# Optimization experiments

Hardware: AMD Instinct MI355X
Metric: run time of the kernel (lower is better)

The kernel has to match this reference:

```python
import jax, jax.numpy as jnp
import numpy as np

B, T, N, D = 8, 512, 64, 128
PRED, HEADS, HID = 96, 8, 256
KERNELS = (17, 49)
NUM_LAYERS = 1
NUM_BLOCKS = 1
IDX_T = np.arange(64)   # lowest 64 of T//2=256 rfft modes (mode_select='low')
IDX_C = np.arange(32)   # min(modes, (N+1)//2)=32 lowest channel-frequency modes


def _mov_avg(x, k):
    # x: [B, T, N]; replicate-pad (k-1)//2 on both ends, then box filter (AvgPool1d stride 1)
    pad = (k - 1) // 2
    xp = jnp.concatenate([jnp.repeat(x[:, :1], pad, axis=1), x, jnp.repeat(x[:, -1:], pad, axis=1)], axis=1)
    c = jnp.cumsum(xp, axis=1)
    c = jnp.concatenate([jnp.zeros_like(c[:, :1]), c], axis=1)
    return (c[:, k:] - c[:, :-k]) / k


def _decomp_multi(x, dec_w, dec_b):
    # series_decomp_multi: softmax-weighted mixture of moving averages
    mm = jnp.stack([_mov_avg(x, k) for k in KERNELS], axis=-1)        # [B,T,N,K]
    w = jax.nn.softmax(x[..., None] * dec_w + dec_b, axis=-1)         # Linear(1,K) on x, softmax over K
    trend = jnp.sum(mm * w, axis=-1)
    return x - trend, trend


def _complex_attn(x, Wq, Wk, Wv, Wo):
    # x: complex64 [B, L, M, D]; multi-head attention over the M selected frequency modes.
    # Real projection weights applied to complex activations; attention weights are
    # softmax over |q k^H| / sqrt(dh); values stay complex.
    Bq, L, M, Dm = x.shape
    dh = Dm // HEADS
    q = jnp.einsum('blmd,de->blme', x, Wq).reshape(Bq, L, M, HEADS, dh)
    k = jnp.einsum('blmd,de->blme', x, Wk).reshape(Bq, L, M, HEADS, dh)
    v = jnp.einsum('blmd,de->blme', x, Wv).reshape(Bq, L, M, HEADS, dh)
    s = jnp.einsum('blmhd,blnhd->blhmn', q, jnp.conj(k))              # complex scores
    w = jax.nn.softmax(jnp.abs(s) / np.sqrt(dh), axis=-1)             # real attn weights
    o = jnp.einsum('blhmn,blnhd->blmhd', w.astype(x.dtype), v).reshape(Bq, L, M, Dm)
    return jnp.einsum('blmd,de->blme', o, Wo)


def _cem(x, Wq, Wk, Wv, Wo):
    # channel-frequency attention; x: [B, N, T, D]
    xp = jnp.transpose(x, (0, 2, 1, 3))                               # [B,T,N,D]
    xf = jnp.fft.rfft(xp, axis=2)                                     # [B,T,N//2+1,D]
    xs = xf[:, :, IDX_C, :]                                           # gather selected modes
    for _ in range(NUM_LAYERS):
        xs = _complex_attn(xs, Wq, Wk, Wv, Wo)
    yf = jnp.zeros((x.shape[0], T, N // 2 + 1, D), dtype=xf.dtype).at[:, :, IDX_C, :].set(xs)
    y = jnp.fft.irfft(yf, n=N, axis=2)
    return jnp.transpose(y, (0, 2, 1, 3))


def _tem(x, Wq, Wk, Wv, Wo):
    # temporal-frequency attention; x: [B, N, T, D]
    xf = jnp.fft.rfft(x, axis=2)                                      # [B,N,T//2+1,D]
    xs = xf[:, :, IDX_T, :]
    for _ in range(NUM_LAYERS):
        xs = _complex_attn(xs, Wq, Wk, Wv, Wo)
    yf = jnp.zeros((x.shape[0], N, T // 2 + 1, D), dtype=xf.dtype).at[:, :, IDX_T, :].set(xs)
    return jnp.fft.irfft(yf, n=T, axis=2)


def setup_inputs() -> dict:
    key = jax.random.key(0)
    ks = jax.random.split(key, 24)
    r = lambda i, shape, s: jax.random.normal(ks[i], shape, jnp.float32) * s
    K = len(KERNELS)
    return {
        'x': jax.random.normal(ks[0], (B, T, N), jnp.float32),
        'embeddings': jax.random.normal(ks[1], (1, D), jnp.float32),
        'dec_w': r(2, (K,), 1.0),
        'dec_b': jnp.zeros((K,), jnp.float32),
        'mlp_w1': r(3, (T, HID), 1.0 / np.sqrt(T)),
        'mlp_b1': jnp.zeros((HID,), jnp.float32),
        'mlp_w2': r(4, (HID, HID), 1.0 / np.sqrt(HID)),
        'mlp_b2': jnp.zeros((HID,), jnp.float32),
        'mlp_w3': r(5, (HID, PRED), 1.0 / np.sqrt(HID)),
        'mlp_b3': jnp.zeros((PRED,), jnp.float32),
        'cem_Wq': r(6, (D, D), 0.02), 'cem_Wk': r(7, (D, D), 0.02),
        'cem_Wv': r(8, (D, D), 0.02), 'cem_Wo': r(9, (D, D), 0.02),
        'tem_Wq': r(10, (D, D), 0.02), 'tem_Wk': r(11, (D, D), 0.02),
        'tem_Wv': r(12, (D, D), 0.02), 'tem_Wo': r(13, (D, D), 0.02),
        'dr_w': r(14, (D, 1), 1.0 / np.sqrt(D)),
        'dr_b': jnp.zeros((1,), jnp.float32),
        'out_w': r(15, (T, PRED), 1.0 / np.sqrt(T)),
        'out_b': jnp.zeros((PRED,), jnp.float32),
        'W_fuse': jnp.ones((2,), jnp.float32),
    }


def reference(x, embeddings, dec_w, dec_b, mlp_w1, mlp_b1, mlp_w2, mlp_b2, mlp_w3, mlp_b3,
              cem_Wq, cem_Wk, cem_Wv, cem_Wo, tem_Wq, tem_Wk, tem_Wv, tem_Wo,
              dr_w, dr_b, out_w, out_b, W_fuse):
    res, trend = _decomp_multi(x, dec_w, dec_b)
    t = jnp.transpose(trend, (0, 2, 1))                               # [B,N,T]
    h = jax.nn.relu(t @ mlp_w1 + mlp_b1)
    h = jax.nn.relu(h @ mlp_w2 + mlp_b2)
    trend_out = jnp.transpose(h @ mlp_w3 + mlp_b3, (0, 2, 1))         # [B,PRED,N]
    # tokenEmb: [B,T,N] -> [B,N,T,1] * [1,D]
    xe = jnp.transpose(res, (0, 2, 1))[..., None] * embeddings[0]      # [B,N,T,D]
    for _ in range(NUM_BLOCKS):
        xe = _cem(xe, cem_Wq, cem_Wk, cem_Wv, cem_Wo)
    for _ in range(NUM_BLOCKS):
        xe = _tem(xe, tem_Wq, tem_Wk, tem_Wv, tem_Wo)
    xr = jnp.einsum('bntd,do->bnto', xe, dr_w)[..., 0] + dr_b[0]      # dim_reduction -> [B,N,T]
    xo = jnp.transpose(jnp.einsum('bnt,tp->bnp', xr, out_w) + out_b, (0, 2, 1))  # [B,PRED,N]
    return W_fuse[0] * xo + W_fuse[1] * trend_out
```

## Files before the change

kernel.cpp:

```cpp
#include <hip/hip_runtime.h>
#include <hip/hip_bf16.h>

typedef __hip_bfloat16 bf16;

constexpr int CB = 8;
constexpr int CT = 512;
constexpr int CN = 64;
constexpr int CD = 128;
constexpr int CP = 96;
constexpr int CH = 8;
constexpr int CDH = 16;
constexpr int CHID = 256;
constexpr int CM = 32;
constexpr int CG = 64;
constexpr float TWO_PI = 6.28318530717958647692f;

__device__ __forceinline__ float LD(const void* p, size_t i, bool f) {
  return f ? ((const float*)p)[i] : __bfloat162float(((const bf16*)p)[i]);
}
template <bool F32>
__device__ __forceinline__ float LDT(const void* p, size_t i) {
  return F32 ? ((const float*)p)[i] : __bfloat162float(((const bf16*)p)[i]);
}

__device__ __forceinline__ bool detect_f32(const void* x) {
  const unsigned int* xw = (const unsigned int*)x;
  unsigned int w = xw[threadIdx.x & 63];
  unsigned int e = (w >> 7) & 0xFF;
  unsigned long long m = __ballot(e >= 0x90 || e <= 0x60);
  return __popcll(m) > 3;
}

__device__ __forceinline__ float2 pkfma(float2 a, float2 b, float2 c) {
  return make_float2(fmaf(a.x, b.x, c.x), fmaf(a.y, b.y, c.y));
}

__global__ __launch_bounds__(256) void kL1(const void* x, const void* dec_w, const void* dec_b,
                                           const void* out_w, const void* emb, const void* cWq,
                                           const void* cWk, const void* cWv, const void* cWo,
                                           const void* tWo, const void* drw,
                                           float* res, float* trend, float* owr, float* owi,
                                           float* g_ch, float* g_ewo, float* g_wod) {
  __shared__ float sm[CT * 17];
  bool f32 = detect_f32(x);
  int blk = blockIdx.x, tid = threadIdx.x;
  if (blk < 32) {
    float (*xl)[17] = (float (*)[17])sm;
    int b = blk >> 2, n0 = (blk & 3) * 16;
    size_t base = (size_t)b * CT * CN + n0;
    for (int i = tid; i < CT * 16; i += 256) {
      int t = i >> 4, j = i & 15;
      xl[t][j] = LD(x, base + (size_t)t * CN + j, f32);
    }
    __syncthreads();
    float w0 = LD(dec_w, 0, f32), w1 = LD(dec_w, 1, f32);
    float c0 = LD(dec_b, 0, f32), c1 = LD(dec_b, 1, f32);
    int j = tid & 15, tl = tid >> 4;
    for (int k = 0; k < CT / 16; ++k) {
      int t = k * 16 + tl;
      float s17 = 0;
      #pragma unroll
      for (int o = -8; o <= 8; ++o) {
        int u = t + o; u = u < 0 ? 0 : (u > CT - 1 ? CT - 1 : u);
        s17 += xl[u][j];
      }
      float s49 = 0;
      #pragma unroll
      for (int o = -24; o <= 24; ++o) {
        int u = t + o; u = u < 0 ? 0 : (u > CT - 1 ? CT - 1 : u);
        s49 += xl[u][j];
      }
      float m0 = s17 * (1.f / 17.f), m1 = s49 * (1.f / 49.f);
      float xv = xl[t][j];
      float l0 = xv * w0 + c0, l1 = xv * w1 + c1;
      float mx = fmaxf(l0, l1);
      float e0 = __expf(l0 - mx), e1 = __expf(l1 - mx);
      float tr = (e0 * m0 + e1 * m1) / (e0 + e1);
      size_t o = ((size_t)(b * CT + t)) * CN + n0 + j;
      trend[o] = tr;
      res[o] = xv - tr;
    }
  } else if (blk < 96) {
    float* twc = sm; float* tws = sm + CT;
    int g = blk - 32;
    for (int t = tid; t < CT; t += 256) {
      int k = (g * t) & (CT - 1);
      float s, c;
      sincosf((float)k * (TWO_PI / CT), &s, &c);
      twc[t] = c; tws[t] = s;
    }
    __syncthreads();
    if (tid < CP) {
      float sr = 0, si = 0;
      #pragma unroll 8
      for (int t = 0; t < CT; ++t) {
        float w = LD(out_w, t * CP + tid, f32);
        sr += w * twc[t]; si += w * tws[t];
      }
      owr[g * CP + tid] = sr; owi[g * CP + tid] = si;
    }
  } else {
    float* eml = sm; float* drl = sm + 128; float* eql = sm + 256;
    float* ekl = sm + 384; float* evl = sm + 512;
    if (tid < 128) eml[tid] = LD(emb, tid, f32);
    else drl[tid - 128] = LD(drw, tid - 128, f32);
    __syncthreads();
    int e = tid & 127;
    for (int pass = 0; pass < 2; ++pass) {
      int grp = pass * 2 + (tid >> 7);
      if (grp < 3) {
        const void* W = grp == 0 ? cWq : (grp == 1 ? cWk : cWv);
        float a = 0;
        #pragma unroll 8
        for (int d = 0; d < CD; ++d) a += eml[d] * LD(W, d * CD + e, f32);
        (grp == 0 ? eql : (grp == 1 ? ekl : evl))[e] = a;
      } else {
        float a = 0;
        #pragma unroll 8
        for (int d = 0; d < CD; ++d) a += LD(tWo, e * CD + d, f32) * drl[d];
        g_wod[e] = a;
      }
    }
    __syncthreads();
    if (tid < CH) {
      float c = 0;
      for (int j = 0; j < CDH; ++j) c += eql[tid * CDH + j] * ekl[tid * CDH + j];
      g_ch[tid] = fabsf(c);
    }
    int half = tid >> 7;
    for (int hh = 0; hh < 4; ++hh) {
      int h = half * 4 + hh;
      float a = 0;
      #pragma unroll
      for (int j = 0; j < CDH; ++j) a += evl[h * CDH + j] * LD(cWo, (h * CDH + j) * CD + e, f32);
      g_ewo[h * CD + e] = a;
    }
  }
}

template <bool F32>
__device__ __forceinline__ void k2_body(float* sm, const float* __restrict__ trend, const void* w1,
                                        const void* bb1, const void* w2, const void* bb2,
                                        const void* w3, const void* bb3,
                                        float* __restrict__ trendo) {
  float* rows = sm;
  float* h1 = sm + 2048;
  float* h2 = sm + 3072;
  int r0 = blockIdx.x * 4;
  int b = r0 >> 6, n0 = r0 & 63;
  int tid = threadIdx.x;
  const float* tb = trend + (size_t)b * CT * CN + n0;
  for (int i = tid; i < 4 * CT; i += 256) {
    int q = i & 3, t = i >> 2;
    rows[q * CT + t] = tb[(size_t)t * CN + q];
  }
  __syncthreads();
  int c = tid;
  float a0, a1, a2, a3;
  {
    float bias = LDT<F32>(bb1, c);
    a0 = a1 = a2 = a3 = 0.f;
    #pragma unroll 16
    for (int t = 0; t < CT; ++t) {
      float w = LDT<F32>(w1, t * CHID + c);
      a0 += rows[0 * CT + t] * w; a1 += rows[1 * CT + t] * w;
      a2 += rows[2 * CT + t] * w; a3 += rows[3 * CT + t] * w;
    }
    h1[0 * CHID + c] = fmaxf(a0 + bias, 0.f); h1[1 * CHID + c] = fmaxf(a1 + bias, 0.f);
    h1[2 * CHID + c] = fmaxf(a2 + bias, 0.f); h1[3 * CHID + c] = fmaxf(a3 + bias, 0.f);
  }
  __syncthreads();
  {
    float bias = LDT<F32>(bb2, c);
    a0 = a1 = a2 = a3 = 0.f;
    #pragma unroll 16
    for (int i = 0; i < CHID; ++i) {
      float w = LDT<F32>(w2, i * CHID + c);
      a0 += h1[0 * CHID + i] * w; a1 += h1[1 * CHID + i] * w;
      a2 += h1[2 * CHID + i] * w; a3 += h1[3 * CHID + i] * w;
    }
    h2[0 * CHID + c] = fmaxf(a0 + bias, 0.f); h2[1 * CHID + c] = fmaxf(a1 + bias, 0.f);
    h2[2 * CHID + c] = fmaxf(a2 + bias, 0.f); h2[3 * CHID + c] = fmaxf(a3 + bias, 0.f);
  }
  __syncthreads();
  if (tid < 2 * CP) {
    int p = tid < CP ? tid : tid - CP;
    int qh = tid < CP ? 0 : 2;
    float bias = LDT<F32>(bb3, p);
    a0 = a1 = 0.f;
    #pragma unroll 16
    for (int i = 0; i < CHID; ++i) {
      float w = LDT<F32>(w3, i * CP + p);
      a0 += h2[qh * CHID + i] * w; a1 += h2[(qh + 1) * CHID + i] * w;
    }
    trendo[((size_t)(b * CN + n0 + qh)) * CP + p] = a0 + bias;
    trendo[((size_t)(b * CN + n0 + qh + 1)) * CP + p] = a1 + bias;
  }
}

__global__ __launch_bounds__(256) void kL2(const void* x, const float* trend, const void* w1,
                                           const void* bb1, const void* w2, const void* bb2,
                                           const void* w3, const void* bb3, float* trendo,
                                           const float* res, const float* g_ch, float* P,
                                           const void* tWq, const void* tWk, const void* tWv,
                                           const float* g_ewo, float* g_ewq, float* g_ewk,
                                           float* g_ewv) {
  __shared__ float sm[4096];
  bool f32 = detect_f32(x);
  int blk = blockIdx.x, tid = threadIdx.x;
  if (blk < 128) {
    if (f32) k2_body<true>(sm, trend, w1, bb1, w2, bb2, w3, bb3, trendo);
    else     k2_body<false>(sm, trend, w1, bb1, w2, bb2, w3, bb3, trendo);
  } else if (blk < 1152) {
    float* rowl = sm;
    float* twc = sm + 256;
    float* tws = sm + 320;
    float* chl = sm + 384;
    float* Rr = sm + 392;
    float* Ri = sm + 520;
    float* aR = sm + 648;
    float* Sr = sm + 776;
    float* Si = sm + 1800;
    int tblk = blk - 128;
    int b = tblk >> 7;
    int w = tid >> 6, lane = tid & 63;
    int t = ((tblk & 127) << 2) + w;
    rowl[w * 64 + lane] = res[((size_t)(b * CT + t)) * CN + lane];
    if (w == 0) {
      float s, c;
      sincosf((float)lane * (TWO_PI / CN), &s, &c);
      twc[lane] = c; tws[lane] = s;
    }
    if (tid < CH) chl[tid] = g_ch[tid];
    __syncthreads();
    if (lane < CM) {
      float rr = 0, ri = 0;
      int idx = 0;
      for (int n2 = 0; n2 < CN; ++n2) {
        rr += rowl[w * 64 + n2] * twc[idx];
        ri -= rowl[w * 64 + n2] * tws[idx];
        idx = (idx + lane) & (CN - 1);
      }
      Rr[w * 32 + lane] = rr; Ri[w * 32 + lane] = ri;
      aR[w * 32 + lane] = sqrtf(rr * rr + ri * ri);
    }
    __syncthreads();
    float amax = 0;
    for (int m = 0; m < CM; ++m) amax = fmaxf(amax, aR[w * 32 + m]);
    for (int i = 0; i < 4; ++i) {
      int pair = lane + 64 * i;
      int h = pair >> 5, m = pair & 31;
      float alpha = 0.25f * chl[h] * aR[w * 32 + m];
      float den = 0, sr = 0, si = 0;
      for (int n2 = 0; n2 < CM; ++n2) {
        float e = __expf(alpha * (aR[w * 32 + n2] - amax));
        den += e; sr += e * Rr[w * 32 + n2]; si += e * Ri[w * 32 + n2];
      }
      Sr[w * 256 + pair] = sr / den; Si[w * 256 + pair] = si / den;
    }
    __syncthreads();
    int n2 = lane;
    float av[8];
    for (int h = 0; h < CH; ++h) {
      float a = Sr[w * 256 + h * CM];
      int idx = n2 & (CN - 1);
      #pragma unroll
      for (int f = 1; f < CM; ++f) {
        a += 2.f * (Sr[w * 256 + h * CM + f] * twc[idx] - Si[w * 256 + h * CM + f] * tws[idx]);
        idx = (idx + n2) & (CN - 1);
      }
      av[h] = a * (1.f / CN);
    }
    float* Pb = P + (((size_t)(b * CN + n2)) * CT + t) * CH;
    ((float4*)Pb)[0] = make_float4(av[0], av[1], av[2], av[3]);
    ((float4*)Pb)[1] = make_float4(av[4], av[5], av[6], av[7]);
  } else {
    float* ew = sm;
    int pairIdx = (blk - 1152) * 2 + (tid >> 7);
    int which = pairIdx >> 3, h = pairIdx & 7, e = tid & 127;
    ew[(tid >> 7) * 128 + e] = g_ewo[h * CD + e];
    __syncthreads();
    const void* W = which == 0 ? tWq : (which == 1 ? tWk : tWv);
    float a = 0;
    #pragma unroll 8
    for (int d = 0; d < CD; ++d) a += ew[(tid >> 7) * 128 + d] * LD(W, d * CD + e, f32);
    (which == 0 ? g_ewq : (which == 1 ? g_ewk : g_ewv))[h * CD + e] = a;
  }
}

__global__ __launch_bounds__(256) void kL3(const float* P, float* Q, const float* g_ewq,
                                           const float* g_ewk, const float* g_ewv,
                                           const float* g_wod, float* g_C, float* g_u) {
  __shared__ float sm[4096];
  int blk = blockIdx.x, tid = threadIdx.x;
  if (blk < 512) {
    float* Pl = sm;
    int b = blk >> 6, n = blk & 63;
    const float4* Pp4 = (const float4*)(P + ((size_t)(b * CN + n)) * CT * CH);
    float4* Pl4 = (float4*)Pl;
    for (int i = tid; i < CT * CH / 4; i += 256) Pl4[i] = Pp4[i];
    __syncthreads();
    int g1 = tid >> 3, h = tid & 7, g2 = g1 + 32;
    float s1, c1, s2, c2;
    sincosf((float)g1 * (TWO_PI / CT), &s1, &c1);
    sincosf((float)g2 * (TWO_PI / CT), &s2, &c2);
    float wr1 = 1.f, wi1 = 0.f, wr2 = 1.f, wi2 = 0.f;
    float r1 = 0, i1 = 0, r2 = 0, i2 = 0;
    #pragma unroll 8
    for (int t = 0; t < CT; ++t) {
      float p = Pl[t * CH + h];
      r1 += p * wr1; i1 += p * wi1;
      r2 += p * wr2; i2 += p * wi2;
      float nr1 = wr1 * c1 + wi1 * s1; wi1 = wi1 * c1 - wr1 * s1; wr1 = nr1;
      float nr2 = wr2 * c2 + wi2 * s2; wi2 = wi2 * c2 - wr2 * s2; wr2 = nr2;
    }
    float* Qb = Q + ((size_t)(b * CN + n)) * CG * CH * 2;
    Qb[(g1 * CH + h) * 2] = r1; Qb[(g1 * CH + h) * 2 + 1] = i1;
    Qb[(g2 * CH + h) * 2] = r2; Qb[(g2 * CH + h) * 2 + 1] = i2;
  } else {
    for (int id = tid; id < 512 + 64; id += 256) {
      if (id < 512) {
        int h = id >> 6, a = (id >> 3) & 7, b2 = id & 7;
        float c = 0;
        #pragma unroll
        for (int j = 0; j < CDH; ++j)
          c += g_ewq[a * CD + h * CDH + j] * g_ewk[b2 * CD + h * CDH + j];
        g_C[id] = c;
      } else {
        int r = id - 512;
        int h = r >> 3, a = r & 7;
        float c = 0;
        #pragma unroll
        for (int j = 0; j < CDH; ++j) c += g_ewv[a * CD + h * CDH + j] * g_wod[h * CDH + j];
        g_u[r] = c;
      }
    }
  }
}

__global__ __launch_bounds__(512) void k5_tem(const void* x, const float* Q, const float* g_C,
                                              const float* g_u, const float* owr,
                                              const float* owi, const float* trendo,
                                              const void* dr_b, const void* out_b,
                                              const void* wfuse, void* out) {
  __shared__ float QL[CG][16];
  __shared__ float Cl[512];
  __shared__ float Ul[CH][8];
  __shared__ float2 vdL[CH][CG];
  __shared__ float2 zL[CH][CG];
  __shared__ float zrow[CG][2];
  bool f32 = detect_f32(x);
  int blk = blockIdx.x;
  int b = blk >> 6, n = blk & 63;
  int tid = threadIdx.x;
  const float* Qb = Q + ((size_t)(b * CN + n)) * CG * CH * 2;
  ((float2*)&QL[0][0])[tid] = ((const float2*)Qb)[tid];
  Cl[tid] = g_C[tid];
  if (tid < 64) ((float*)Ul)[tid] = g_u[tid];
  __syncthreads();
  int h = tid >> 6, m = tid & 63;
  float2 qp[8];
  {
    const float4* q4 = (const float4*)QL[m];
    #pragma unroll
    for (int j = 0; j < 4; ++j) {
      float4 y = q4[j];
      qp[2 * j] = make_float2(y.x, y.y);
      qp[2 * j + 1] = make_float2(y.z, y.w);
    }
  }
  {
    float vr = 0, vi = 0;
    #pragma unroll
    for (int a = 0; a < 8; ++a) { float u = Ul[h][a]; vr += qp[a].x * u; vi += qp[a].y * u; }
    vdL[h][m] = make_float2(vr, vi);
  }
  float2 uu[8], vv[8];
  #pragma unroll
  for (int bb = 0; bb < 8; ++bb) {
    float sr = 0, si = 0;
    #pragma unroll
    for (int a = 0; a < 8; ++a) {
      float c = Cl[(h * 8 + a) * 8 + bb];
      sr += qp[a].x * c; si += qp[a].y * c;
    }
    uu[bb] = make_float2(sr, si);
    vv[bb] = make_float2(si, -sr);
  }
  __syncthreads();
  float mx = -1e30f, den = 0.f, zr = 0.f, zi = 0.f;
  #pragma unroll 4
  for (int g = 0; g < CG; ++g) {
    const float4* k4p = (const float4*)QL[g];
    float2 sr2 = make_float2(0.f, 0.f), si2 = make_float2(0.f, 0.f);
    #pragma unroll
    for (int j = 0; j < 4; ++j) {
      float4 y = k4p[j];
      float2 y0 = make_float2(y.x, y.y), y1 = make_float2(y.z, y.w);
      sr2 = pkfma(uu[2 * j], y0, sr2); si2 = pkfma(vv[2 * j], y0, si2);
      sr2 = pkfma(uu[2 * j + 1], y1, sr2); si2 = pkfma(vv[2 * j + 1], y1, si2);
    }
    float sr = sr2.x + sr2.y;
    float si = si2.x + si2.y;
    float s = 0.25f * sqrtf(sr * sr + si * si);
    if (s > mx) {
      float f = __expf(mx - s);
      den *= f; zr *= f; zi *= f; mx = s;
    }
    float e = __expf(s - mx);
    float2 vd = vdL[h][g];
    den += e; zr += e * vd.x; zi += e * vd.y;
  }
  float rv = 1.f / den;
  zL[h][m] = make_float2(zr * rv, zi * rv);
  __syncthreads();
  if (tid < 128) {
    int g = tid >> 1, c = tid & 1;
    float a = 0;
    #pragma unroll
    for (int hh = 0; hh < CH; ++hh) a += c ? zL[hh][g].y : zL[hh][g].x;
    zrow[g][c] = a;
  }
  __syncthreads();
  if (tid < CP) {
    int p = tid;
    float acc = zrow[0][0] * owr[p] - zrow[0][1] * owi[p];
    #pragma unroll 8
    for (int g = 1; g < CG; ++g)
      acc += 2.f * (zrow[g][0] * owr[g * CP + p] - zrow[g][1] * owi[g * CP + p]);
    float xo = acc * (1.f / CT) + LD(dr_b, 0, f32) * owr[p] + LD(out_b, p, f32);
    float val = LD(wfuse, 0, f32) * xo + LD(wfuse, 1, f32) * trendo[((size_t)(b * CN + n)) * CP + p];
    size_t oidx = ((size_t)(b * CP + p)) * CN + n;
    if (f32) ((float*)out)[oidx] = val;
    else ((bf16*)out)[oidx] = __float2bfloat16(val);
  }
}

extern "C" void kernel_launch(void* const* d_in, const int* in_sizes, int n_in,
                              void* d_out, int out_size, void* d_ws, size_t ws_size,
                              hipStream_t stream) {
  const void* x = d_in[0];
  const void* emb = d_in[1];
  const void* dec_w = d_in[2];
  const void* dec_b = d_in[3];
  const void* mlp_w1 = d_in[4];
  const void* mlp_b1 = d_in[5];
  const void* mlp_w2 = d_in[6];
  const void* mlp_b2 = d_in[7];
  const void* mlp_w3 = d_in[8];
  const void* mlp_b3 = d_in[9];
  const void* cWq = d_in[10];
  const void* cWk = d_in[11];
  const void* cWv = d_in[12];
  const void* cWo = d_in[13];
  const void* tWq = d_in[14];
  const void* tWk = d_in[15];
  const void* tWv = d_in[16];
  const void* tWo = d_in[17];
  const void* drw = d_in[18];
  const void* drb = d_in[19];
  const void* out_w = d_in[20];
  const void* out_b = d_in[21];
  const void* wfuse = d_in[22];

  float* W = (float*)d_ws;
  float* res = W;    W += (size_t)CB * CT * CN;
  float* trend = W;  W += (size_t)CB * CT * CN;
  float* trendo = W; W += (size_t)CB * CN * CP;
  float* Pbuf = W;   W += (size_t)CB * CT * CH * CN;
  float* Qbuf = W;   W += (size_t)CB * CN * CG * CH * 2;
  float* ch = W;     W += 8;
  float* ewo = W;    W += CH * CD;
  float* ewq = W;    W += CH * CD;
  float* ewk = W;    W += CH * CD;
  float* ewv = W;    W += CH * CD;
  float* wod = W;    W += CD;
  float* owr = W;    W += CG * CP;
  float* owi = W;    W += CG * CP;
  float* gC = W;     W += 512;
  float* gU = W;     W += 64;

  kL1<<<97, 256, 0, stream>>>(x, dec_w, dec_b, out_w, emb, cWq, cWk, cWv, cWo, tWo, drw,
                              res, trend, owr, owi, ch, ewo, wod);
  kL2<<<1164, 256, 0, stream>>>(x, trend, mlp_w1, mlp_b1, mlp_w2, mlp_b2, mlp_w3, mlp_b3,
                                trendo, res, ch, Pbuf, tWq, tWk, tWv, ewo, ewq, ewk, ewv);
  kL3<<<513, 256, 0, stream>>>(Pbuf, Qbuf, ewq, ewk, ewv, wod, gC, gU);
  k5_tem<<<CB * CN, 512, 0, stream>>>(x, Qbuf, gC, gU, owr, owi, trendo, drb, out_b, wfuse,
                                      d_out);
}
```

Before: 226.3 us.

## Fuse four kernels into one cooperative persistent kernel with grid syncs

```diff
diff --git a/kernel.cpp b/kernel.cpp
--- a/kernel.cpp
+++ b/kernel.cpp
@@ -1,6 +1,8 @@
 #include <hip/hip_runtime.h>
+#include <hip/hip_cooperative_groups.h>
 #include <hip/hip_bf16.h>
 
+namespace cg = cooperative_groups;
 typedef __hip_bfloat16 bf16;
 
 constexpr int CB = 8;
@@ -35,121 +37,132 @@
   return make_float2(fmaf(a.x, b.x, c.x), fmaf(a.y, b.y, c.y));
 }
 
-__global__ __launch_bounds__(256) void kL1(const void* x, const void* dec_w, const void* dec_b,
-                                           const void* out_w, const void* emb, const void* cWq,
-                                           const void* cWk, const void* cWv, const void* cWo,
-                                           const void* tWo, const void* drw,
-                                           float* res, float* trend, float* owr, float* owi,
-                                           float* g_ch, float* g_ewo, float* g_wod) {
-  __shared__ float sm[CT * 17];
-  bool f32 = detect_f32(x);
-  int blk = blockIdx.x, tid = threadIdx.x;
+struct MArgs {
+  const void *x, *dec_w, *dec_b, *out_w, *emb, *cWq, *cWk, *cWv, *cWo;
+  const void *tWq, *tWk, *tWv, *tWo, *drw, *drb, *out_b, *wfuse;
+  const void *w1, *b1, *w2, *b2, *w3, *b3;
+  float *res, *trend, *trendo, *Pbuf, *Qbuf, *ch, *ewo, *ewq, *ewk, *ewv, *wod;
+  float *owr, *owi, *gC, *gU;
+  void* out;
+};
+
+__device__ void stage1(const MArgs& a, float* sm, bool f32, int blk, int tid) {
   if (blk < 32) {
-    float (*xl)[17] = (float (*)[17])sm;
+    float* xl = sm;
     int b = blk >> 2, n0 = (blk & 3) * 16;
     size_t base = (size_t)b * CT * CN + n0;
     for (int i = tid; i < CT * 16; i += 256) {
       int t = i >> 4, j = i & 15;
-      xl[t][j] = LD(x, base + (size_t)t * CN + j, f32);
-    }
-    __syncthreads();
-    float w0 = LD(dec_w, 0, f32), w1 = LD(dec_w, 1, f32);
-    float c0 = LD(dec_b, 0, f32), c1 = LD(dec_b, 1, f32);
+      xl[t * 16 + j] = LD(a.x, base + (size_t)t * CN + j, f32);
+    }
+    __syncthreads();
+    float w0 = LD(a.dec_w, 0, f32), w1 = LD(a.dec_w, 1, f32);
+    float c0 = LD(a.dec_b, 0, f32), c1 = LD(a.dec_b, 1, f32);
     int j = tid & 15, tl = tid >> 4;
-    for (int k = 0; k < CT / 16; ++k) {
-      int t = k * 16 + tl;
-      float s17 = 0;
-      #pragma unroll
-      for (int o = -8; o <= 8; ++o) {
-        int u = t + o; u = u < 0 ? 0 : (u > CT - 1 ? CT - 1 : u);
-        s17 += xl[u][j];
-      }
-      float s49 = 0;
-      #pragma unroll
-      for (int o = -24; o <= 24; ++o) {
-        int u = t + o; u = u < 0 ? 0 : (u > CT - 1 ? CT - 1 : u);
-        s49 += xl[u][j];
+    int t0 = tl * 32;
+    float s17 = 0.f, s49 = 0.f;
+    #pragma unroll
+    for (int o = -8; o <= 8; ++o) {
+      int u = t0 + o; u = u < 0 ? 0 : (u > CT - 1 ? CT - 1 : u);
+      s17 += xl[u * 16 + j];
+    }
+    #pragma unroll
+    for (int o = -24; o <= 24; ++o) {
+      int u = t0 + o; u = u < 0 ? 0 : (u > CT - 1 ? CT - 1 : u);
+      s49 += xl[u * 16 + j];
+    }
+    for (int k = 0; k < 32; ++k) {
+      int t = t0 + k;
+      if (k > 0) {
+        int up8 = t + 8 > CT - 1 ? CT - 1 : t + 8;
+        int dn9 = t - 9 < 0 ? 0 : t - 9;
+        int up24 = t + 24 > CT - 1 ? CT - 1 : t + 24;
+        int dn25 = t - 25 < 0 ? 0 : t - 25;
+        s17 += xl[up8 * 16 + j] - xl[dn9 * 16 + j];
+        s49 += xl[up24 * 16 + j] - xl[dn25 * 16 + j];
       }
       float m0 = s17 * (1.f / 17.f), m1 = s49 * (1.f / 49.f);
-      float xv = xl[t][j];
+      float xv = xl[t * 16 + j];
       float l0 = xv * w0 + c0, l1 = xv * w1 + c1;
       float mx = fmaxf(l0, l1);
       float e0 = __expf(l0 - mx), e1 = __expf(l1 - mx);
       float tr = (e0 * m0 + e1 * m1) / (e0 + e1);
       size_t o = ((size_t)(b * CT + t)) * CN + n0 + j;
-      trend[o] = tr;
-      res[o] = xv - tr;
+      a.trend[o] = tr;
+      a.res[o] = xv - tr;
     }
   } else if (blk < 96) {
-    float* twc = sm; float* tws = sm + CT;
+    float* ps = sm;
     int g = blk - 32;
-    for (int t = tid; t < CT; t += 256) {
-      int k = (g * t) & (CT - 1);
-      float s, c;
-      sincosf((float)k * (TWO_PI / CT), &s, &c);
-      twc[t] = c; tws[t] = s;
+    int tc = tid >> 7, idx = tid & 127;
+    if (idx < CP) {
+      int p = idx, t0 = tc * 256;
+      float s0, c0v, ss, cs;
+      sincosf((float)((g * t0) & (CT - 1)) * (TWO_PI / CT), &s0, &c0v);
+      sincosf((float)g * (TWO_PI / CT), &ss, &cs);
+      float wr = c0v, wi = s0, ar = 0.f, ai = 0.f;
+      #pragma unroll 16
+      for (int t = 0; t < 256; ++t) {
+        float w = LD(a.out_w, (size_t)(t0 + t) * CP + p, f32);
+        ar = fmaf(w, wr, ar); ai = fmaf(w, wi, ai);
+        float nr = wr * cs - wi * ss; wi = wi * cs + wr * ss; wr = nr;
+      }
+      ps[(tc * CP + p) * 2] = ar; ps[(tc * CP + p) * 2 + 1] = ai;
     }
     __syncthreads();
     if (tid < CP) {
-      float sr = 0, si = 0;
-      #pragma unroll 8
-      for (int t = 0; t < CT; ++t) {
-        float w = LD(out_w, t * CP + tid, f32);
-        sr += w * twc[t]; si += w * tws[t];
-      }
-      owr[g * CP + tid] = sr; owi[g * CP + tid] = si;
-    }
-  } else {
+      a.owr[g * CP + tid] = ps[tid * 2] + ps[(CP + tid) * 2];
+      a.owi[g * CP + tid] = ps[tid * 2 + 1] + ps[(CP + tid) * 2 + 1];
+    }
+  } else if (blk == 96) {
     float* eml = sm; float* drl = sm + 128; float* eql = sm + 256;
     float* ekl = sm + 384; float* evl = sm + 512;
-    if (tid < 128) eml[tid] = LD(emb, tid, f32);
-    else drl[tid - 128] = LD(drw, tid - 128, f32);
+    if (tid < 128) eml[tid] = LD(a.emb, tid, f32);
+    else drl[tid - 128] = LD(a.drw, tid - 128, f32);
     __syncthreads();
     int e = tid & 127;
     for (int pass = 0; pass < 2; ++pass) {
       int grp = pass * 2 + (tid >> 7);
       if (grp < 3) {
-        const void* W = grp == 0 ? cWq : (grp == 1 ? cWk : cWv);
-        float a = 0;
-        #pragma unroll 8
-        for (int d = 0; d < CD; ++d) a += eml[d] * LD(W, d * CD + e, f32);
-        (grp == 0 ? eql : (grp == 1 ? ekl : evl))[e] = a;
+        const void* W = grp == 0 ? a.cWq : (grp == 1 ? a.cWk : a.cWv);
+        float acc = 0;
+        #pragma unroll 16
+        for (int d = 0; d < CD; ++d) acc += eml[d] * LD(W, d * CD + e, f32);
+        (grp == 0 ? eql : (grp == 1 ? ekl : evl))[e] = acc;
       } else {
-        float a = 0;
-        #pragma unroll 8
-        for (int d = 0; d < CD; ++d) a += LD(tWo, e * CD + d, f32) * drl[d];
-        g_wod[e] = a;
+        float acc = 0;
+        #pragma unroll 16
+        for (int d = 0; d < CD; ++d) acc += LD(a.tWo, e * CD + d, f32) * drl[d];
+        a.wod[e] = acc;
       }
     }
     __syncthreads();
     if (tid < CH) {
       float c = 0;
       for (int j = 0; j < CDH; ++j) c += eql[tid * CDH + j] * ekl[tid * CDH + j];
-      g_ch[tid] = fabsf(c);
+      a.ch[tid] = fabsf(c);
     }
     int half = tid >> 7;
     for (int hh = 0; hh < 4; ++hh) {
       int h = half * 4 + hh;
-      float a = 0;
+      float acc = 0;
       #pragma unroll
-      for (int j = 0; j < CDH; ++j) a += evl[h * CDH + j] * LD(cWo, (h * CDH + j) * CD + e, f32);
-      g_ewo[h * CD + e] = a;
+      for (int j = 0; j < CDH; ++j)
+        acc += evl[h * CDH + j] * LD(a.cWo, (h * CDH + j) * CD + e, f32);
+      a.ewo[h * CD + e] = acc;
     }
   }
 }
 
 template <bool F32>
-__device__ __forceinline__ void k2_body(float* sm, const float* __restrict__ trend, const void* w1,
-                                        const void* bb1, const void* w2, const void* bb2,
-                                        const void* w3, const void* bb3,
-                                        float* __restrict__ trendo) {
+__device__ void k2_body(float* sm, const MArgs& a) {
   float* rows = sm;
   float* h1 = sm + 2048;
   float* h2 = sm + 3072;
   int r0 = blockIdx.x * 4;
   int b = r0 >> 6, n0 = r0 & 63;
   int tid = threadIdx.x;
-  const float* tb = trend + (size_t)b * CT * CN + n0;
+  const float* tb = a.trend + (size_t)b * CT * CN + n0;
   for (int i = tid; i < 4 * CT; i += 256) {
     int q = i & 3, t = i >> 2;
     rows[q * CT + t] = tb[(size_t)t * CN + q];
@@ -158,11 +171,11 @@
   int c = tid;
   float a0, a1, a2, a3;
   {
-    float bias = LDT<F32>(bb1, c);
+    float bias = LDT<F32>(a.b1, c);
     a0 = a1 = a2 = a3 = 0.f;
     #pragma unroll 16
     for (int t = 0; t < CT; ++t) {
-      float w = LDT<F32>(w1, t * CHID + c);
+      float w = LDT<F32>(a.w1, t * CHID + c);
       a0 += rows[0 * CT + t] * w; a1 += rows[1 * CT + t] * w;
       a2 += rows[2 * CT + t] * w; a3 += rows[3 * CT + t] * w;
     }
@@ -171,11 +184,11 @@
   }
   __syncthreads();
   {
-    float bias = LDT<F32>(bb2, c);
+    float bias = LDT<F32>(a.b2, c);
     a0 = a1 = a2 = a3 = 0.f;
     #pragma unroll 16
     for (int i = 0; i < CHID; ++i) {
-      float w = LDT<F32>(w2, i * CHID + c);
+      float w = LDT<F32>(a.w2, i * CHID + c);
       a0 += h1[0 * CHID + i] * w; a1 += h1[1 * CHID + i] * w;
       a2 += h1[2 * CHID + i] * w; a3 += h1[3 * CHID + i] * w;
     }
@@ -186,32 +199,23 @@
   if (tid < 2 * CP) {
     int p = tid < CP ? tid : tid - CP;
     int qh = tid < CP ? 0 : 2;
-    float bias = LDT<F32>(bb3, p);
+    float bias = LDT<F32>(a.b3, p);
     a0 = a1 = 0.f;
     #pragma unroll 16
     for (int i = 0; i < CHID; ++i) {
-      float w = LDT<F32>(w3, i * CP + p);
+      float w = LDT<F32>(a.w3, i * CP + p);
       a0 += h2[qh * CHID + i] * w; a1 += h2[(qh + 1) * CHID + i] * w;
     }
-    trendo[((size_t)(b * CN + n0 + qh)) * CP + p] = a0 + bias;
-    trendo[((size_t)(b * CN + n0 + qh + 1)) * CP + p] = a1 + bias;
-  }
-}
-
-__global__ __launch_bounds__(256) void kL2(const void* x, const float* trend, const void* w1,
-                                           const void* bb1, const void* w2, const void* bb2,
-                                           const void* w3, const void* bb3, float* trendo,
-                                           const float* res, const float* g_ch, float* P,
-                                           const void* tWq, const void* tWk, const void* tWv,
-                                           const float* g_ewo, float* g_ewq, float* g_ewk,
-                                           float* g_ewv) {
-  __shared__ float sm[4096];
-  bool f32 = detect_f32(x);
-  int blk = blockIdx.x, tid = threadIdx.x;
+    a.trendo[((size_t)(b * CN + n0 + qh)) * CP + p] = a0 + bias;
+    a.trendo[((size_t)(b * CN + n0 + qh + 1)) * CP + p] = a1 + bias;
+  }
+}
+
+__device__ void stage2(const MArgs& a, float* sm, bool f32, int blk, int tid) {
   if (blk < 128) {
-    if (f32) k2_body<true>(sm, trend, w1, bb1, w2, bb2, w3, bb3, trendo);
-    else     k2_body<false>(sm, trend, w1, bb1, w2, bb2, w3, bb3, trendo);
-  } else if (blk < 1152) {
+    if (f32) k2_body<true>(sm, a);
+    else     k2_body<false>(sm, a);
+  } else if (blk < 1012) {
     float* rowl = sm;
     float* twc = sm + 256;
     float* tws = sm + 320;
@@ -221,82 +225,85 @@
     float* aR = sm + 648;
     float* Sr = sm + 776;
     float* Si = sm + 1800;
-    int tblk = blk - 128;
-    int b = tblk >> 7;
+    int bk = blk - 128;
+    int iters = bk < 140 ? 2 : 1;
+    int tbase = bk < 140 ? bk * 8 : 140 * 8 + (bk - 140) * 4;
     int w = tid >> 6, lane = tid & 63;
-    int t = ((tblk & 127) << 2) + w;
-    rowl[w * 64 + lane] = res[((size_t)(b * CT + t)) * CN + lane];
     if (w == 0) {
       float s, c;
       sincosf((float)lane * (TWO_PI / CN), &s, &c);
       twc[lane] = c; tws[lane] = s;
     }
-    if (tid < CH) chl[tid] = g_ch[tid];
-    __syncthreads();
-    if (lane < CM) {
-      float rr = 0, ri = 0;
-      int idx = 0;
-      for (int n2 = 0; n2 < CN; ++n2) {
-        rr += rowl[w * 64 + n2] * twc[idx];
-        ri -= rowl[w * 64 + n2] * tws[idx];
-        idx = (idx + lane) & (CN - 1);
-      }
-      Rr[w * 32 + lane] = rr; Ri[w * 32 + lane] = ri;
-      aR[w * 32 + lane] = sqrtf(rr * rr + ri * ri);
-    }
-    __syncthreads();
-    float amax = 0;
-    for (int m = 0; m < CM; ++m) amax = fmaxf(amax, aR[w * 32 + m]);
-    for (int i = 0; i < 4; ++i) {
-      int pair = lane + 64 * i;
-      int h = pair >> 5, m = pair & 31;
-      float alpha = 0.25f * chl[h] * aR[w * 32 + m];
-      float den = 0, sr = 0, si = 0;
-      for (int n2 = 0; n2 < CM; ++n2) {
-        float e = __expf(alpha * (aR[w * 32 + n2] - amax));
-        den += e; sr += e * Rr[w * 32 + n2]; si += e * Ri[w * 32 + n2];
-      }
-      Sr[w * 256 + pair] = sr / den; Si[w * 256 + pair] = si / den;
-    }
-    __syncthreads();
-    int n2 = lane;
-    float av[8];
-    for (int h = 0; h < CH; ++h) {
-      float a = Sr[w * 256 + h * CM];
-      int idx = n2 & (CN - 1);
-      #pragma unroll
-      for (int f = 1; f < CM; ++f) {
-        a += 2.f * (Sr[w * 256 + h * CM + f] * twc[idx] - Si[w * 256 + h * CM + f] * tws[idx]);
-        idx = (idx + n2) & (CN - 1);
-      }
-      av[h] = a * (1.f / CN);
-    }
-    float* Pb = P + (((size_t)(b * CN + n2)) * CT + t) * CH;
-    ((float4*)Pb)[0] = make_float4(av[0], av[1], av[2], av[3]);
-    ((float4*)Pb)[1] = make_float4(av[4], av[5], av[6], av[7]);
+    if (tid < CH) chl[tid] = a.ch[tid];
+    __syncthreads();
+    for (int it = 0; it < iters; ++it) {
+      int task = tbase + it * 4 + w;
+      int b = task >> 9, t = task & 511;
+      rowl[w * 64 + lane] = a.res[((size_t)(b * CT + t)) * CN + lane];
+      __syncthreads();
+      if (lane < CM) {
+        float rr = 0, ri = 0;
+        int idx = 0;
+        for (int n2 = 0; n2 < CN; ++n2) {
+          rr += rowl[w * 64 + n2] * twc[idx];
+          ri -= rowl[w * 64 + n2] * tws[idx];
+          idx = (idx + lane) & (CN - 1);
+        }
+        Rr[w * 32 + lane] = rr; Ri[w * 32 + lane] = ri;
+        aR[w * 32 + lane] = sqrtf(rr * rr + ri * ri);
+      }
+      __syncthreads();
+      float amax = 0;
+      for (int m = 0; m < CM; ++m) amax = fmaxf(amax, aR[w * 32 + m]);
+      for (int i = 0; i < 4; ++i) {
+        int pair = lane + 64 * i;
+        int h = pair >> 5, m = pair & 31;
+        float alpha = 0.25f * chl[h] * aR[w * 32 + m];
+        float den = 0, sr = 0, si = 0;
+        for (int n2 = 0; n2 < CM; ++n2) {
+          float e = __expf(alpha * (aR[w * 32 + n2] - amax));
+          den += e; sr += e * Rr[w * 32 + n2]; si += e * Ri[w * 32 + n2];
+        }
+        Sr[w * 256 + pair] = sr / den; Si[w * 256 + pair] = si / den;
+      }
+      __syncthreads();
+      int n2 = lane;
+      float av[8];
+      for (int h = 0; h < CH; ++h) {
+        float acc = Sr[w * 256 + h * CM];
+        int idx = n2 & (CN - 1);
+        #pragma unroll
+        for (int f = 1; f < CM; ++f) {
+          acc += 2.f * (Sr[w * 256 + h * CM + f] * twc[idx]
+                      - Si[w * 256 + h * CM + f] * tws[idx]);
+          idx = (idx + n2) & (CN - 1);
+        }
+        av[h] = acc * (1.f / CN);
+      }
+      float* Pb = a.Pbuf + (((size_t)(b * CN + n2)) * CT + t) * CH;
+      ((float4*)Pb)[0] = make_float4(av[0], av[1], av[2], av[3]);
+      ((float4*)Pb)[1] = make_float4(av[4], av[5], av[6], av[7]);
+      __syncthreads();
+    }
   } else {
     float* ew = sm;
-    int pairIdx = (blk - 1152) * 2 + (tid >> 7);
+    int pairIdx = (blk - 1012) * 2 + (tid >> 7);
     int which = pairIdx >> 3, h = pairIdx & 7, e = tid & 127;
-    ew[(tid >> 7) * 128 + e] = g_ewo[h * CD + e];
-    __syncthreads();
-    const void* W = which == 0 ? tWq : (which == 1 ? tWk : tWv);
-    float a = 0;
-    #pragma unroll 8
-    for (int d = 0; d < CD; ++d) a += ew[(tid >> 7) * 128 + d] * LD(W, d * CD + e, f32);
-    (which == 0 ? g_ewq : (which == 1 ? g_ewk : g_ewv))[h * CD + e] = a;
-  }
-}
-
-__global__ __launch_bounds__(256) void kL3(const float* P, float* Q, const float* g_ewq,
-                                           const float* g_ewk, const float* g_ewv,
-                                           const float* g_wod, float* g_C, float* g_u) {
-  __shared__ float sm[4096];
-  int blk = blockIdx.x, tid = threadIdx.x;
+    ew[(tid >> 7) * 128 + e] = a.ewo[h * CD + e];
+    __syncthreads();
+    const void* W = which == 0 ? a.tWq : (which == 1 ? a.tWk : a.tWv);
+    float acc = 0;
+    #pragma unroll 16
+    for (int d = 0; d < CD; ++d) acc += ew[(tid >> 7) * 128 + d] * LD(W, d * CD + e, f32);
+    (which == 0 ? a.ewq : (which == 1 ? a.ewk : a.ewv))[h * CD + e] = acc;
+  }
+}
+
+__device__ void stage3(const MArgs& a, float* sm, bool f32, int blk, int tid) {
   if (blk < 512) {
     float* Pl = sm;
     int b = blk >> 6, n = blk & 63;
-    const float4* Pp4 = (const float4*)(P + ((size_t)(b * CN + n)) * CT * CH);
+    const float4* Pp4 = (const float4*)(a.Pbuf + ((size_t)(b * CN + n)) * CT * CH);
     float4* Pl4 = (float4*)Pl;
     for (int i = tid; i < CT * CH / 4; i += 256) Pl4[i] = Pp4[i];
     __syncthreads();
@@ -314,54 +321,48 @@
       float nr1 = wr1 * c1 + wi1 * s1; wi1 = wi1 * c1 - wr1 * s1; wr1 = nr1;
       float nr2 = wr2 * c2 + wi2 * s2; wi2 = wi2 * c2 - wr2 * s2; wr2 = nr2;
     }
-    float* Qb = Q + ((size_t)(b * CN + n)) * CG * CH * 2;
+    float* Qb = a.Qbuf + ((size_t)(b * CN + n)) * CG * CH * 2;
     Qb[(g1 * CH + h) * 2] = r1; Qb[(g1 * CH + h) * 2 + 1] = i1;
     Qb[(g2 * CH + h) * 2] = r2; Qb[(g2 * CH + h) * 2 + 1] = i2;
-  } else {
+  } else if (blk == 512) {
     for (int id = tid; id < 512 + 64; id += 256) {
       if (id < 512) {
-        int h = id >> 6, a = (id >> 3) & 7, b2 = id & 7;
+        int h = id >> 6, aa = (id >> 3) & 7, b2 = id & 7;
         float c = 0;
         #pragma unroll
         for (int j = 0; j < CDH; ++j)
-          c += g_ewq[a * CD + h * CDH + j] * g_ewk[b2 * CD + h * CDH + j];
-        g_C[id] = c;
+          c += a.ewq[aa * CD + h * CDH + j] * a.ewk[b2 * CD + h * CDH + j];
+        a.gC[id] = c;
       } else {
         int r = id - 512;
-        int h = r >> 3, a = r & 7;
+        int h = r >> 3, aa = r & 7;
         float c = 0;
         #pragma unroll
-        for (int j = 0; j < CDH; ++j) c += g_ewv[a * CD + h * CDH + j] * g_wod[h * CDH + j];
-        g_u[r] = c;
-      }
-    }
-  }
-}
-
-__global__ __launch_bounds__(512) void k5_tem(const void* x, const float* Q, const float* g_C,
-                                              const float* g_u, const float* owr,
-                                              const float* owi, const float* trendo,
-                                              const void* dr_b, const void* out_b,
-                                              const void* wfuse, void* out) {
-  __shared__ float QL[CG][16];
-  __shared__ float Cl[512];
-  __shared__ float Ul[CH][8];
-  __shared__ float2 vdL[CH][CG];
-  __shared__ float2 zL[CH][CG];
-  __shared__ float zrow[CG][2];
-  bool f32 = detect_f32(x);
-  int blk = blockIdx.x;
+        for (int j = 0; j < CDH; ++j) c += a.ewv[aa * CD + h * CDH + j] * a.wod[h * CDH + j];
+        a.gU[r] = c;
+      }
+    }
+  }
+}
+
+__device__ void stage4(const MArgs& a, float* sm, bool f32, int blk, int tid) {
+  if (blk >= 512) return;
+  float* QL = sm;
+  float* Cl = sm + 1024;
+  float* Ul = sm + 1536;
+  float2* vdL = (float2*)(sm + 1600);
+  float2* zL = (float2*)(sm + 2624);
+  float* zrow = sm + 3648;
   int b = blk >> 6, n = blk & 63;
-  int tid = threadIdx.x;
-  const float* Qb = Q + ((size_t)(b * CN + n)) * CG * CH * 2;
-  ((float2*)&QL[0][0])[tid] = ((const float2*)Qb)[tid];
-  Cl[tid] = g_C[tid];
-  if (tid < 64) ((float*)Ul)[tid] = g_u[tid];
-  __syncthreads();
-  int h = tid >> 6, m = tid & 63;
+  const float* Qb = a.Qbuf + ((size_t)(b * CN + n)) * CG * CH * 2;
+  for (int i = tid; i < 512; i += 256) ((float4*)QL)[i] = ((const float4*)Qb)[i];
+  for (int i = tid; i < 512; i += 256) Cl[i] = a.gC[i];
+  if (tid < 64) Ul[tid] = a.gU[tid];
+  __syncthreads();
+  int h0 = tid >> 6, m = tid & 63;
   float2 qp[8];
   {
-    const float4* q4 = (const float4*)QL[m];
+    const float4* q4 = (const float4*)(QL + m * 16);
     #pragma unroll
     for (int j = 0; j < 4; ++j) {
       float4 y = q4[j];
@@ -369,122 +370,149 @@
       qp[2 * j + 1] = make_float2(y.z, y.w);
     }
   }
-  {
+  #pragma unroll
+  for (int e2 = 0; e2 < 2; ++e2) {
+    int hh = h0 + e2 * 4;
     float vr = 0, vi = 0;
     #pragma unroll
-    for (int a = 0; a < 8; ++a) { float u = Ul[h][a]; vr += qp[a].x * u; vi += qp[a].y * u; }
-    vdL[h][m] = make_float2(vr, vi);
-  }
-  float2 uu[8], vv[8];
-  #pragma unroll
-  for (int bb = 0; bb < 8; ++bb) {
-    float sr = 0, si = 0;
+    for (int aa = 0; aa < 8; ++aa) {
+      float u = Ul[hh * 8 + aa];
+      vr += qp[aa].x * u; vi += qp[aa].y * u;
+    }
+    vdL[hh * 64 + m] = make_float2(vr, vi);
+  }
+  __syncthreads();
+  for (int e2 = 0; e2 < 2; ++e2) {
+    int hh = h0 + e2 * 4;
+    float2 uu[8], vv[8];
     #pragma unroll
-    for (int a = 0; a < 8; ++a) {
-      float c = Cl[(h * 8 + a) * 8 + bb];
-      sr += qp[a].x * c; si += qp[a].y * c;
-    }
-    uu[bb] = make_float2(sr, si);
-    vv[bb] = make_float2(si, -sr);
-  }
-  __syncthreads();
-  float mx = -1e30f, den = 0.f, zr = 0.f, zi = 0.f;
-  #pragma unroll 4
-  for (int g = 0; g < CG; ++g) {
-    const float4* k4p = (const float4*)QL[g];
-    float2 sr2 = make_float2(0.f, 0.f), si2 = make_float2(0.f, 0.f);
-    #pragma unroll
-    for (int j = 0; j < 4; ++j) {
-      float4 y = k4p[j];
-      float2 y0 = make_float2(y.x, y.y), y1 = make_float2(y.z, y.w);
-      sr2 = pkfma(uu[2 * j], y0, sr2); si2 = pkfma(vv[2 * j], y0, si2);
-      sr2 = pkfma(uu[2 * j + 1], y1, sr2); si2 = pkfma(vv[2 * j + 1], y1, si2);
-    }
-    float sr = sr2.x + sr2.y;
-    float si = si2.x + si2.y;
-    float s = 0.25f * sqrtf(sr * sr + si * si);
-    if (s > mx) {
-      float f = __expf(mx - s);
-      den *= f; zr *= f; zi *= f; mx = s;
-    }
-    float e = __expf(s - mx);
-    float2 vd = vdL[h][g];
-    den += e; zr += e * vd.x; zi += e * vd.y;
-  }
-  float rv = 1.f / den;
-  zL[h][m] = make_float2(zr * rv, zi * rv);
+    for (int bb = 0; bb < 8; ++bb) {
+      float sr = 0, si = 0;
+      #pragma unroll
+      for (int aa = 0; aa < 8; ++aa) {
+        float c = Cl[(hh * 8 + aa) * 8 + bb];
+        sr += qp[aa].x * c; si += qp[aa].y * c;
+      }
+      uu[bb] = make_float2(sr, si);
+      vv[bb] = make_float2(si, -sr);
+    }
+    float mx = -1e30f, den = 0.f, zr = 0.f, zi = 0.f;
+    #pragma unroll 4
+    for (int g = 0; g < CG; ++g) {
+      const float4* k4p = (const float4*)(QL + g * 16);
+      float2 sr2 = make_float2(0.f, 0.f), si2 = make_float2(0.f, 0.f);
+      #pragma unroll
+      for (int j = 0; j < 4; ++j) {
+        float4 y = k4p[j];
+        float2 y0 = make_float2(y.x, y.y), y1 = make_float2(y.z, y.w);
+        sr2 = pkfma(uu[2 * j], y0, sr2); si2 = pkfma(vv[2 * j], y0, si2);
+        sr2 = pkfma(uu[2 * j + 1], y1, sr2); si2 = pkfma(vv[2 * j + 1], y1, si2);
+      }
+      float sr = sr2.x + sr2.y;
+      float si = si2.x + si2.y;
+      float s = 0.25f * sqrtf(sr * sr + si * si);
+      if (s > mx) {
+        float f = __expf(mx - s);
+        den *= f; zr *= f; zi *= f; mx = s;
+      }
+      float e = __expf(s - mx);
+      float2 vd = vdL[hh * 64 + g];
+      den += e; zr += e * vd.x; zi += e * vd.y;
+    }
+    float rv = 1.f / den;
+    zL[hh * 64 + m] = make_float2(zr * rv, zi * rv);
+  }
   __syncthreads();
   if (tid < 128) {
     int g = tid >> 1, c = tid & 1;
-    float a = 0;
+    float acc = 0;
     #pragma unroll
-    for (int hh = 0; hh < CH; ++hh) a += c ? zL[hh][g].y : zL[hh][g].x;
-    zrow[g][c] = a;
+    for (int hh = 0; hh < CH; ++hh) acc += c ? zL[hh * 64 + g].y : zL[hh * 64 + g].x;
+    zrow[g * 2 + c] = acc;
   }
   __syncthreads();
   if (tid < CP) {
     int p = tid;
-    float acc = zrow[0][0] * owr[p] - zrow[0][1] * owi[p];
+    float acc = zrow[0] * a.owr[p] - zrow[1] * a.owi[p];
     #pragma unroll 8
     for (int g = 1; g < CG; ++g)
-      acc += 2.f * (zrow[g][0] * owr[g * CP + p] - zrow[g][1] * owi[g * CP + p]);
-    float xo = acc * (1.f / CT) + LD(dr_b, 0, f32) * owr[p] + LD(out_b, p, f32);
-    float val = LD(wfuse, 0, f32) * xo + LD(wfuse, 1, f32) * trendo[((size_t)(b * CN + n)) * CP + p];
+      acc += 2.f * (zrow[g * 2] * a.owr[g * CP + p] - zrow[g * 2 + 1] * a.owi[g * CP + p]);
+    float xo = acc * (1.f / CT) + LD(a.drb, 0, f32) * a.owr[p] + LD(a.out_b, p, f32);
+    float val = LD(a.wfuse, 0, f32) * xo
+              + LD(a.wfuse, 1, f32) * a.trendo[((size_t)(b * CN + n)) * CP + p];
     size_t oidx = ((size_t)(b * CP + p)) * CN + n;
-    if (f32) ((float*)out)[oidx] = val;
-    else ((bf16*)out)[oidx] = __float2bfloat16(val);
-  }
+    if (f32) ((float*)a.out)[oidx] = val;
+    else ((bf16*)a.out)[oidx] = __float2bfloat16(val);
+  }
+}
+
+__global__ __launch_bounds__(256, 4) void mega(MArgs a) {
+  __shared__ __align__(16) float sm[8192];
+  bool f32 = detect_f32(a.x);
+  int blk = blockIdx.x, tid = threadIdx.x;
+  cg::grid_group grid = cg::this_grid();
+  stage1(a, sm, f32, blk, tid);
+  grid.sync();
+  stage2(a, sm, f32, blk, tid);
+  grid.sync();
+  stage3(a, sm, f32, blk, tid);
+  grid.sync();
+  stage4(a, sm, f32, blk, tid);
+}
+
+__global__ __launch_bounds__(256, 4) void gs1(MArgs a) {
+  __shared__ __align__(16) float sm[8192];
+  stage1(a, sm, detect_f32(a.x), blockIdx.x, threadIdx.x);
+}
+__global__ __launch_bounds__(256, 4) void gs2(MArgs a) {
+  __shared__ __align__(16) float sm[8192];
+  stage2(a, sm, detect_f32(a.x), blockIdx.x, threadIdx.x);
+}
+__global__ __launch_bounds__(256, 4) void gs3(MArgs a) {
+  __shared__ __align__(16) float sm[8192];
+  stage3(a, sm, detect_f32(a.x), blockIdx.x, threadIdx.x);
+}
+__global__ __launch_bounds__(256, 4) void gs4(MArgs a) {
+  __shared__ __align__(16) float sm[8192];
+  stage4(a, sm, detect_f32(a.x), blockIdx.x, threadIdx.x);
 }
 
 extern "C" void kernel_launch(void* const* d_in, const int* in_sizes, int n_in,
                               void* d_out, int out_size, void* d_ws, size_t ws_size,
                               hipStream_t stream) {
-  const void* x = d_in[0];
-  const void* emb = d_in[1];
-  const void* dec_w = d_in[2];
-  const void* dec_b = d_in[3];
-  const void* mlp_w1 = d_in[4];
-  const void* mlp_b1 = d_in[5];
-  const void* mlp_w2 = d_in[6];
-  const void* mlp_b2 = d_in[7];
-  const void* mlp_w3 = d_in[8];
-  const void* mlp_b3 = d_in[9];
-  const void* cWq = d_in[10];
-  const void* cWk = d_in[11];
-  const void* cWv = d_in[12];
-  const void* cWo = d_in[13];
-  const void* tWq = d_in[14];
-  const void* tWk = d_in[15];
-  const void* tWv = d_in[16];
-  const void* tWo = d_in[17];
-  const void* drw = d_in[18];
-  const void* drb = d_in[19];
-  const void* out_w = d_in[20];
-  const void* out_b = d_in[21];
-  const void* wfuse = d_in[22];
-
   float* W = (float*)d_ws;
-  float* res = W;    W += (size_t)CB * CT * CN;
-  float* trend = W;  W += (size_t)CB * CT * CN;
-  float* trendo = W; W += (size_t)CB * CN * CP;
-  float* Pbuf = W;   W += (size_t)CB * CT * CH * CN;
-  float* Qbuf = W;   W += (size_t)CB * CN * CG * CH * 2;
-  float* ch = W;     W += 8;
-  float* ewo = W;    W += CH * CD;
-  float* ewq = W;    W += CH * CD;
-  float* ewk = W;    W += CH * CD;
-  float* ewv = W;    W += CH * CD;
-  float* wod = W;    W += CD;
-  float* owr = W;    W += CG * CP;
-  float* owi = W;    W += CG * CP;
-  float* gC = W;     W += 512;
-  float* gU = W;     W += 64;
-
-  kL1<<<97, 256, 0, stream>>>(x, dec_w, dec_b, out_w, emb, cWq, cWk, cWv, cWo, tWo, drw,
-                              res, trend, owr, owi, ch, ewo, wod);
-  kL2<<<1164, 256, 0, stream>>>(x, trend, mlp_w1, mlp_b1, mlp_w2, mlp_b2, mlp_w3, mlp_b3,
-                                trendo, res, ch, Pbuf, tWq, tWk, tWv, ewo, ewq, ewk, ewv);
-  kL3<<<513, 256, 0, stream>>>(Pbuf, Qbuf, ewq, ewk, ewv, wod, gC, gU);
-  k5_tem<<<CB * CN, 512, 0, stream>>>(x, Qbuf, gC, gU, owr, owi, trendo, drb, out_b, wfuse,
-                                      d_out);
-}
+  MArgs a;
+  a.x = d_in[0];   a.emb = d_in[1];  a.dec_w = d_in[2]; a.dec_b = d_in[3];
+  a.w1 = d_in[4];  a.b1 = d_in[5];   a.w2 = d_in[6];    a.b2 = d_in[7];
+  a.w3 = d_in[8];  a.b3 = d_in[9];
+  a.cWq = d_in[10]; a.cWk = d_in[11]; a.cWv = d_in[12]; a.cWo = d_in[13];
+  a.tWq = d_in[14]; a.tWk = d_in[15]; a.tWv = d_in[16]; a.tWo = d_in[17];
+  a.drw = d_in[18]; a.drb = d_in[19]; a.out_w = d_in[20]; a.out_b = d_in[21];
+  a.wfuse = d_in[22];
+  a.res = W;    W += (size_t)CB * CT * CN;
+  a.trend = W;  W += (size_t)CB * CT * CN;
+  a.trendo = W; W += (size_t)CB * CN * CP;
+  a.Pbuf = W;   W += (size_t)CB * CT * CH * CN;
+  a.Qbuf = W;   W += (size_t)CB * CN * CG * CH * 2;
+  a.ch = W;     W += 8;
+  a.ewo = W;    W += CH * CD;
+  a.ewq = W;    W += CH * CD;
+  a.ewk = W;    W += CH * CD;
+  a.ewv = W;    W += CH * CD;
+  a.wod = W;    W += CD;
+  a.owr = W;    W += CG * CP;
+  a.owi = W;    W += CG * CP;
+  a.gC = W;     W += 512;
+  a.gU = W;     W += 64;
+  a.out = d_out;
+
+  void* kargs[] = { &a };
+  hipError_t err = hipLaunchCooperativeKernel(reinterpret_cast<void*>(mega),
+                                              dim3(1024), dim3(256), kargs, 0, stream);
+  if (err != hipSuccess) {
+    gs1<<<1024, 256, 0, stream>>>(a);
+    gs2<<<1024, 256, 0, stream>>>(a);
+    gs3<<<1024, 256, 0, stream>>>(a);
+    gs4<<<1024, 256, 0, stream>>>(a);
+  }
+}
```

After: 584.0 us. 158% more time.
